# Performance work log

Measured on AMD Instinct MI355X. Metric: run time of the kernel, lower is better.

Reference implementation:

```python
import jax, jax.numpy as jnp
import numpy as np

I1, H1, H2, NC = 38, 50, 15, 14

def _lstm(x, w_ih, w_hh, b_ih, b_hh):
    # x: [B, T, I]; weights in torch layout: w_ih [4H, I], w_hh [4H, H]
    # torch gate order: i, f, g, o
    B, T, _ = x.shape
    H = w_hh.shape[1]
    gx = jnp.einsum('bti,gi->btg', x, w_ih) + b_ih + b_hh  # [B, T, 4H]
    gx = jnp.swapaxes(gx, 0, 1)  # [T, B, 4H]

    def step(carry, g_t):
        h, c = carry
        g = g_t + h @ w_hh.T
        i_g, f_g, c_g, o_g = jnp.split(g, 4, axis=-1)
        i_g = jax.nn.sigmoid(i_g)
        f_g = jax.nn.sigmoid(f_g)
        o_g = jax.nn.sigmoid(o_g)
        c = f_g * c + i_g * jnp.tanh(c_g)
        h = o_g * jnp.tanh(c)
        return (h, c), h

    init = (jnp.zeros((B, H), x.dtype), jnp.zeros((B, H), x.dtype))
    _, hs = jax.lax.scan(step, init, gx)  # hs: [T, B, H]
    return jnp.swapaxes(hs, 0, 1)  # [B, T, H]

def setup_inputs() -> dict:
    key = jax.random.key(0)
    ks = jax.random.split(key, 12)
    s1 = 1.0 / np.sqrt(H1)
    s2 = 1.0 / np.sqrt(H2)
    u = lambda k, shape, s: jax.random.uniform(k, shape, jnp.float32, -s, s)
    return {
        'x': jax.random.normal(ks[0], (4096, 256, I1), jnp.float32),
        'w_ih1': u(ks[1], (4 * H1, I1), s1),
        'w_hh1': u(ks[2], (4 * H1, H1), s1),
        'b_ih1': u(ks[3], (4 * H1,), s1),
        'b_hh1': u(ks[4], (4 * H1,), s1),
        'w_ih2': u(ks[5], (4 * H2, H1), s2),
        'w_hh2': u(ks[6], (4 * H2, H2), s2),
        'b_ih2': u(ks[7], (4 * H2,), s2),
        'b_hh2': u(ks[8], (4 * H2,), s2),
        'w_fc': u(ks[9], (NC, H2), s2),
        'b_fc': u(ks[10], (NC,), s2),
    }

def reference(x, w_ih1, w_hh1, b_ih1, b_hh1, w_ih2, w_hh2, b_ih2, b_hh2, w_fc, b_fc):
    out = _lstm(x, w_ih1, w_hh1, b_ih1, b_hh1)          # [B, T, 50]
    # dropout(0.2) is identity in eval mode
    out = _lstm(out, w_ih2, w_hh2, b_ih2, b_hh2)        # [B, T, 15]
    return out[:, -1, :] @ w_fc.T + b_fc                # [B, 14]
```

## Files before the change

### kernel.cpp

```cpp
#include <hip/hip_runtime.h>


typedef _Float16 f16x8 __attribute__((ext_vector_type(8)));
typedef _Float16 f16x4 __attribute__((ext_vector_type(4)));
typedef float    f32x4 __attribute__((ext_vector_type(4)));

#if __has_builtin(__builtin_amdgcn_exp2f)
#define DEV_EXP2(x) __builtin_amdgcn_exp2f(x)
#else
#define DEV_EXP2(x) exp2f(x)
#endif
#if __has_builtin(__builtin_amdgcn_rcpf)
#define DEV_RCP(x) __builtin_amdgcn_rcpf(x)
#else
#define DEV_RCP(x) (1.0f/(x))
#endif

#define I1 38
#define H1 50
#define H2 15
#define NC 14
#define TT 256
#define SB 16
#define XS 136
#define NTH 512
#define WROW 304
#define L2E 2.885390081777927f
#define L1E 1.442695040888963f

#define MF(A,B,C) __builtin_amdgcn_mfma_f32_16x16x32_f16((A),(B),(C),0,0,0)

__device__ __forceinline__ float sigm(float v)  { return DEV_RCP(1.f + DEV_EXP2(-L1E * v)); }
__device__ __forceinline__ float tanh_f(float v){ return 1.f - 2.f * DEV_RCP(1.f + DEV_EXP2(L2E * v)); }

__launch_bounds__(NTH, 1)
__global__ void lstm2_fused(const float* __restrict__ x,
                            const float* __restrict__ w_ih1, const float* __restrict__ w_hh1,
                            const float* __restrict__ b_ih1, const float* __restrict__ b_hh1,
                            const float* __restrict__ w_ih2, const float* __restrict__ w_hh2,
                            const float* __restrict__ b_ih2, const float* __restrict__ b_hh2,
                            const float* __restrict__ w_fc, const float* __restrict__ b_fc,
                            float* __restrict__ out)
{
  __shared__ __align__(16) _Float16 bufA[2][SB][XS];
  __shared__ __align__(16) _Float16 s_win[2][SB][WROW];

  const int tid  = threadIdx.x;
  const int wv   = tid >> 6;
  const int lane = tid & 63;
  const int lm   = lane & 15;
  const int lk   = lane >> 4;
  const int blk  = blockIdx.x;
  const float* xblk = x + (size_t)blk * SB * TT * I1;

  for (int i = tid; i < 2*SB*XS; i += NTH) ((_Float16*)bufA)[i] = (_Float16)0.f;

  auto welem = [&](bool il1, bool valid, int u, int g, int k) -> _Float16 {
    float w = 0.f;
    if (valid) {
      if (il1) {
        if (k < I1)                w = w_ih1[(g*H1 + u)*I1 + k];
        else if (k < I1 + H1)      w = w_hh1[(g*H1 + u)*H1 + (k - I1)];
      } else {
        if (k >= I1 && k < I1+H1)             w = w_ih2[(g*H2 + u)*H1 + (k - I1)];
        else if (k >= I1+H1 && k < I1+H1+H2)  w = w_hh2[(g*H2 + u)*H2 + (k - I1 - H1)];
      }
    }
    return (_Float16)w;
  };

  const int t1 = wv + 8;
  const int r0 = wv*16 + lm, u0f = r0 >> 2, g0 = r0 & 3;
  const int r1 = t1*16 + lm, q1 = r1 >> 2, g1 = r1 & 3;
  const bool il1f = (q1 < H1);
  const int  u1f = il1f ? q1 : (q1 - H1);
  const bool w16 = (wv == 0);
  const bool c16 = w16 && (lm < 4);

  f16x8 W0[3], W1[4], W16[3];
  #pragma unroll
  for (int ks = 0; ks < 3; ++ks) {
    f16x8 v;
    #pragma unroll
    for (int e = 0; e < 8; ++e) v[e] = welem(true, true, u0f, g0, ks*32 + lk*8 + e);
    W0[ks] = v;
  }
  #pragma unroll
  for (int ks = 0; ks < 4; ++ks) {
    f16x8 v;
    #pragma unroll
    for (int e = 0; e < 8; ++e) v[e] = welem(il1f, true, u1f, g1, ks*32 + lk*8 + e);
    W1[ks] = v;
  }
  #pragma unroll
  for (int j = 0; j < 3; ++j) {
    f16x8 v;
    #pragma unroll
    for (int e = 0; e < 8; ++e) v[e] = welem(false, c16, 14, lm & 3, (j+1)*32 + lk*8 + e);
    W16[j] = v;
  }

  const int uS0 = 4*wv + lk;
  const int d0  = 38 + uS0;
  const int uS1 = 32 + 4*wv + lk;
  const bool il1u = (uS1 < H1);
  const int  uS1r = il1u ? uS1 : (uS1 - H1);
  const int  d1   = il1u ? (38 + uS1) : (88 + uS1r);
  const bool hasC = w16 && (lk == 0);

  float sb0[4], sb1[4], sbC[4];
  #pragma unroll
  for (int m = 0; m < 4; ++m) {
    sb0[m] = b_ih1[m*H1 + uS0] + b_hh1[m*H1 + uS0];
    sb1[m] = il1u ? (b_ih1[m*H1 + uS1] + b_hh1[m*H1 + uS1])
                  : (b_ih2[m*H2 + uS1r] + b_hh2[m*H2 + uS1r]);
    sbC[m] = b_ih2[m*H2 + 14] + b_hh2[m*H2 + 14];
  }

  auto load_window = [&](int t0, int buf) {
    #pragma unroll
    for (int it = 0; it < 3; ++it) {
      int c = it*NTH + tid;
      if (c < SB*76) {
        int s = c / 76, r = c % 76;
        const float4 v = *(const float4*)(xblk + (size_t)s*(TT*I1) + t0*I1 + 4*r);
        f16x4 h;
        h[0] = (_Float16)v.x; h[1] = (_Float16)v.y;
        h[2] = (_Float16)v.z; h[3] = (_Float16)v.w;
        *(f16x4*)&s_win[buf][s][4*r] = h;
      }
    }
  };

  const int e1x = tid + 512;
  const bool v1 = (tid < SB*I1 - 512);
  const int s0 = tid / I1,  k0 = tid % I1;
  const int s1 = e1x / I1,  k1 = e1x % I1;
  const int lb0 = s0*XS + k0, lb1 = v1 ? (s1*XS + k1) : 0;

  load_window(0, 0);
  load_window(8, 1);
  __syncthreads();
  {
    _Float16* b0 = &bufA[0][0][0];
    b0[lb0] = s_win[0][s0][k0];
    if (v1) b0[lb1] = s_win[0][s1][k1];
  }
  __syncthreads();

  float cS0 = 0.f, cS1 = 0.f, cC = 0.f;

  for (int t = 0; t <= TT; ++t) {
    _Float16* cur = &bufA[t & 1][0][0];
    _Float16* nxt = &bufA[(t & 1) ^ 1][0][0];

    if ((t & 7) == 7 && t + 9 < TT)
      load_window(t + 9, ((t + 9) >> 3) & 1);

    f16x8 a0 = *(const f16x8*)(cur + lm*XS +      lk*8);
    f16x8 a1 = *(const f16x8*)(cur + lm*XS + 32 + lk*8);
    f16x8 a2 = *(const f16x8*)(cur + lm*XS + 64 + lk*8);
    f16x8 a3 = *(const f16x8*)(cur + lm*XS + 96 + lk*8);

    {
      f32x4 acc = (f32x4){sb0[0], sb0[1], sb0[2], sb0[3]};
      acc = MF(W0[0], a0, acc);
      acc = MF(W0[1], a1, acc);
      acc = MF(W0[2], a2, acc);
      if (t < TT) {
        float ig = sigm(acc[0]), fg = sigm(acc[1]);
        float gg = tanh_f(acc[2]), og = sigm(acc[3]);
        cS0 = fg*cS0 + ig*gg;
        nxt[lm*XS + d0] = (_Float16)(og * tanh_f(cS0));
      }
    }
    {
      f32x4 acc = (f32x4){sb1[0], sb1[1], sb1[2], sb1[3]};
      acc = MF(W1[0], a0, acc);
      acc = MF(W1[1], a1, acc);
      acc = MF(W1[2], a2, acc);
      acc = MF(W1[3], a3, acc);
      const bool up = il1u ? (t < TT) : (t >= 1);
      if (up) {
        float ig = sigm(acc[0]), fg = sigm(acc[1]);
        float gg = tanh_f(acc[2]), og = sigm(acc[3]);
        cS1 = fg*cS1 + ig*gg;
        nxt[lm*XS + d1] = (_Float16)(og * tanh_f(cS1));
      }
    }
    if (w16) {
      f32x4 acc = (f32x4){sbC[0], sbC[1], sbC[2], sbC[3]};
      acc = MF(W16[0], a1, acc);
      acc = MF(W16[1], a2, acc);
      acc = MF(W16[2], a3, acc);
      if (hasC && t >= 1) {
        float ig = sigm(acc[0]), fg = sigm(acc[1]);
        float gg = tanh_f(acc[2]), og = sigm(acc[3]);
        cC = fg*cC + ig*gg;
        nxt[lm*XS + 102] = (_Float16)(og * tanh_f(cC));
      }
    }

    if (t + 1 < TT) {
      const int tw = (t + 1) & 7, bw = ((t + 1) >> 3) & 1;
      nxt[lb0] = s_win[bw][s0][tw*I1 + k0];
      if (v1) nxt[lb1] = s_win[bw][s1][tw*I1 + k1];
    }

    __syncthreads();
  }

  if (tid < SB*NC) {
    int s = tid / NC, n = tid % NC;
    float acc = b_fc[n];
    #pragma unroll
    for (int u = 0; u < H2; ++u)
      acc += (float)bufA[1][s][88 + u] * w_fc[n*H2 + u];
    out[((size_t)blk*SB + s)*NC + n] = acc;
  }
}

extern "C" void kernel_launch(void* const* d_in, const int* in_sizes, int n_in,
                              void* d_out, int out_size, void* d_ws, size_t ws_size,
                              hipStream_t stream) {
  (void)n_in; (void)d_ws; (void)ws_size; (void)out_size;
  const float* x     = (const float*)d_in[0];
  const float* w_ih1 = (const float*)d_in[1];
  const float* w_hh1 = (const float*)d_in[2];
  const float* b_ih1 = (const float*)d_in[3];
  const float* b_hh1 = (const float*)d_in[4];
  const float* w_ih2 = (const float*)d_in[5];
  const float* w_hh2 = (const float*)d_in[6];
  const float* b_ih2 = (const float*)d_in[7];
  const float* b_hh2 = (const float*)d_in[8];
  const float* w_fc  = (const float*)d_in[9];
  const float* b_fc  = (const float*)d_in[10];
  float* out = (float*)d_out;

  const int B = in_sizes[0] / (TT * I1);
  dim3 grid(B / SB), block(NTH);
  lstm2_fused<<<grid, block, 0, stream>>>(x, w_ih1, w_hh1, b_ih1, b_hh1,
                                          w_ih2, w_hh2, b_ih2, b_hh2,
                                          w_fc, b_fc, out);
}
```

Baseline: 201.8 us.

## Double threads per block, one hidden unit per lane, read x directly from window

The block grows from 512 to 1024 threads, so each wave computes one 16-row gate tile instead of two. This roughly halves the serial MFMA and activation chain per timestep. The per-step copy of x from the staging window into the operand buffer is removed. MFMA A operands are now read straight from a padded x window and a separate hidden-state buffer, and waves skip K-slices that are all zero. The trade-off is more waves synchronising at every step's barrier and the launch bound no longer fixing one block per CU.

```diff
diff --git a/kernel.cpp b/kernel.cpp
--- a/kernel.cpp
+++ b/kernel.cpp
@@ -2,7 +2,7 @@
 
 
 typedef _Float16 f16x8 __attribute__((ext_vector_type(8)));
-typedef _Float16 f16x4 __attribute__((ext_vector_type(4)));
+typedef _Float16 f16x2 __attribute__((ext_vector_type(2)));
 typedef float    f32x4 __attribute__((ext_vector_type(4)));
 
 #if __has_builtin(__builtin_amdgcn_exp2f)
@@ -22,9 +22,12 @@
 #define NC 14
 #define TT 256
 #define SB 16
-#define XS 136
-#define NTH 512
-#define WROW 304
+#define NTH 1024
+#define WSR 328
+#define HS  88
+#define WIN_SZ (2*SB*WSR)
+#define H_OFF  WIN_SZ
+#define SMEM_N (WIN_SZ + 2*SB*HS)
 #define L2E 2.885390081777927f
 #define L1E 1.442695040888963f
 
@@ -33,7 +36,7 @@
 __device__ __forceinline__ float sigm(float v)  { return DEV_RCP(1.f + DEV_EXP2(-L1E * v)); }
 __device__ __forceinline__ float tanh_f(float v){ return 1.f - 2.f * DEV_RCP(1.f + DEV_EXP2(L2E * v)); }
 
-__launch_bounds__(NTH, 1)
+__launch_bounds__(NTH)
 __global__ void lstm2_fused(const float* __restrict__ x,
                             const float* __restrict__ w_ih1, const float* __restrict__ w_hh1,
                             const float* __restrict__ b_ih1, const float* __restrict__ b_hh1,
@@ -42,150 +45,116 @@
                             const float* __restrict__ w_fc, const float* __restrict__ b_fc,
                             float* __restrict__ out)
 {
-  __shared__ __align__(16) _Float16 bufA[2][SB][XS];
-  __shared__ __align__(16) _Float16 s_win[2][SB][WROW];
+  __shared__ __align__(16) _Float16 smem[SMEM_N];
 
   const int tid  = threadIdx.x;
   const int wv   = tid >> 6;
   const int lane = tid & 63;
   const int lm   = lane & 15;
-  const int lk   = lane >> 4;
+  const int lkq  = lane >> 4;
   const int blk  = blockIdx.x;
   const float* xblk = x + (size_t)blk * SB * TT * I1;
 
-  for (int i = tid; i < 2*SB*XS; i += NTH) ((_Float16*)bufA)[i] = (_Float16)0.f;
+  for (int i = tid; i < SMEM_N/2; i += NTH) ((int*)smem)[i] = 0;
 
   auto welem = [&](bool il1, bool valid, int u, int g, int k) -> _Float16 {
     float w = 0.f;
     if (valid) {
       if (il1) {
-        if (k < I1)                w = w_ih1[(g*H1 + u)*I1 + k];
-        else if (k < I1 + H1)      w = w_hh1[(g*H1 + u)*H1 + (k - I1)];
+        if (k < I1)                 w = w_ih1[(g*H1 + u)*I1 + k];
+        else if (k >= 40 && k < 90) w = w_hh1[(g*H1 + u)*H1 + (k - 40)];
       } else {
-        if (k >= I1 && k < I1+H1)             w = w_ih2[(g*H2 + u)*H1 + (k - I1)];
-        else if (k >= I1+H1 && k < I1+H1+H2)  w = w_hh2[(g*H2 + u)*H2 + (k - I1 - H1)];
+        if (k >= 40 && k < 90)        w = w_ih2[(g*H2 + u)*H1 + (k - 40)];
+        else if (k >= 90 && k < 105)  w = w_hh2[(g*H2 + u)*H2 + (k - 90)];
       }
     }
     return (_Float16)w;
   };
 
-  const int t1 = wv + 8;
-  const int r0 = wv*16 + lm, u0f = r0 >> 2, g0 = r0 & 3;
-  const int r1 = t1*16 + lm, q1 = r1 >> 2, g1 = r1 & 3;
-  const bool il1f = (q1 < H1);
-  const int  u1f = il1f ? q1 : (q1 - H1);
-  const bool w16 = (wv == 0);
-  const bool c16 = w16 && (lm < 4);
-
-  f16x8 W0[3], W1[4], W16[3];
-  #pragma unroll
-  for (int ks = 0; ks < 3; ++ks) {
-    f16x8 v;
-    #pragma unroll
-    for (int e = 0; e < 8; ++e) v[e] = welem(true, true, u0f, g0, ks*32 + lk*8 + e);
-    W0[ks] = v;
-  }
+  const int quadW = 4*wv + (lm >> 2);
+  const int gW = lm & 3;
+  const bool il1W = (quadW < H1);
+  const int uW = il1W ? quadW : (quadW - H1);
+
+  f16x8 W[4];
   #pragma unroll
   for (int ks = 0; ks < 4; ++ks) {
     f16x8 v;
     #pragma unroll
-    for (int e = 0; e < 8; ++e) v[e] = welem(il1f, true, u1f, g1, ks*32 + lk*8 + e);
-    W1[ks] = v;
-  }
+    for (int e = 0; e < 8; ++e) v[e] = welem(il1W, true, uW, gW, ks*32 + lkq*8 + e);
+    W[ks] = v;
+  }
+  const bool w16 = (wv == 15);
+  const bool c16 = w16 && (lm < 4);
+  f16x8 W16[3];
   #pragma unroll
   for (int j = 0; j < 3; ++j) {
     f16x8 v;
     #pragma unroll
-    for (int e = 0; e < 8; ++e) v[e] = welem(false, c16, 14, lm & 3, (j+1)*32 + lk*8 + e);
+    for (int e = 0; e < 8; ++e) v[e] = welem(false, c16, 14, lm & 3, (j+1)*32 + lkq*8 + e);
     W16[j] = v;
   }
 
-  const int uS0 = 4*wv + lk;
-  const int d0  = 38 + uS0;
-  const int uS1 = 32 + 4*wv + lk;
-  const bool il1u = (uS1 < H1);
-  const int  uS1r = il1u ? uS1 : (uS1 - H1);
-  const int  d1   = il1u ? (38 + uS1) : (88 + uS1r);
-  const bool hasC = w16 && (lk == 0);
-
-  float sb0[4], sb1[4], sbC[4];
+  const int uU = 4*wv + lkq;
+  const bool il1U = (uU < H1);
+  float sb[4], sbC[4];
   #pragma unroll
   for (int m = 0; m < 4; ++m) {
-    sb0[m] = b_ih1[m*H1 + uS0] + b_hh1[m*H1 + uS0];
-    sb1[m] = il1u ? (b_ih1[m*H1 + uS1] + b_hh1[m*H1 + uS1])
-                  : (b_ih2[m*H2 + uS1r] + b_hh2[m*H2 + uS1r]);
+    sb[m] = il1U ? (b_ih1[m*H1 + uU] + b_hh1[m*H1 + uU])
+                 : (b_ih2[m*H2 + (uU - H1)] + b_hh2[m*H2 + (uU - H1)]);
     sbC[m] = b_ih2[m*H2 + 14] + b_hh2[m*H2 + 14];
   }
 
-  auto load_window = [&](int t0, int buf) {
+  __syncthreads();
+
+  auto fill = [&](int t0, int wb) {
     #pragma unroll
     for (int it = 0; it < 3; ++it) {
-      int c = it*NTH + tid;
-      if (c < SB*76) {
-        int s = c / 76, r = c % 76;
-        const float4 v = *(const float4*)(xblk + (size_t)s*(TT*I1) + t0*I1 + 4*r);
-        f16x4 h;
-        h[0] = (_Float16)v.x; h[1] = (_Float16)v.y;
-        h[2] = (_Float16)v.z; h[3] = (_Float16)v.w;
-        *(f16x4*)&s_win[buf][s][4*r] = h;
+      int e = it*NTH + tid;
+      if (e < SB*152) {
+        int s = e / 152, r = e % 152, tw = r / 19, q = r % 19;
+        const float2 v = *(const float2*)(xblk + (size_t)s*TT*I1 + (t0 + tw)*I1 + 2*q);
+        f16x2 h; h[0] = (_Float16)v.x; h[1] = (_Float16)v.y;
+        *(f16x2*)&smem[wb*(SB*WSR) + s*WSR + tw*40 + 2*q] = h;
       }
     }
   };
-
-  const int e1x = tid + 512;
-  const bool v1 = (tid < SB*I1 - 512);
-  const int s0 = tid / I1,  k0 = tid % I1;
-  const int s1 = e1x / I1,  k1 = e1x % I1;
-  const int lb0 = s0*XS + k0, lb1 = v1 ? (s1*XS + k1) : 0;
-
-  load_window(0, 0);
-  load_window(8, 1);
+  fill(0, 0);
+  fill(8, 1);
   __syncthreads();
-  {
-    _Float16* b0 = &bufA[0][0][0];
-    b0[lb0] = s_win[0][s0][k0];
-    if (v1) b0[lb1] = s_win[0][s1][k1];
-  }
-  __syncthreads();
-
-  float cS0 = 0.f, cS1 = 0.f, cC = 0.f;
+
+  float cU = 0.f, cC = 0.f;
 
   for (int t = 0; t <= TT; ++t) {
-    _Float16* cur = &bufA[t & 1][0][0];
-    _Float16* nxt = &bufA[(t & 1) ^ 1][0][0];
-
-    if ((t & 7) == 7 && t + 9 < TT)
-      load_window(t + 9, ((t + 9) >> 3) & 1);
-
-    f16x8 a0 = *(const f16x8*)(cur + lm*XS +      lk*8);
-    f16x8 a1 = *(const f16x8*)(cur + lm*XS + 32 + lk*8);
-    f16x8 a2 = *(const f16x8*)(cur + lm*XS + 64 + lk*8);
-    f16x8 a3 = *(const f16x8*)(cur + lm*XS + 96 + lk*8);
+    const int par = t & 1;
+    const _Float16* curh = smem + H_OFF + par*(SB*HS);
+    _Float16*       nxth = smem + H_OFF + (par ^ 1)*(SB*HS);
+    const _Float16* wint = smem + ((t >> 3) & 1)*(SB*WSR) + (t & 7)*40;
+
+    if ((t & 7) == 0 && t >= 8 && t + 8 < TT)
+      fill(t + 8, ((t >> 3) + 1) & 1);
+
+    f16x8 a0 = (f16x8)(_Float16)0.f;
+    if (wv <= 12) a0 = *(const f16x8*)(wint + lm*WSR + lkq*8);
+    const _Float16* p1 = lkq ? (curh + lm*HS + (lkq*8 - 8))
+                             : (wint + lm*WSR + 32);
+    f16x8 a1 = *(const f16x8*)p1;
+    f16x8 a2 = *(const f16x8*)(curh + lm*HS + 24 + lkq*8);
+    f16x8 a3 = (f16x8)(_Float16)0.f;
+    if (wv >= 12) a3 = *(const f16x8*)(curh + lm*HS + 56 + lkq*8);
 
     {
-      f32x4 acc = (f32x4){sb0[0], sb0[1], sb0[2], sb0[3]};
-      acc = MF(W0[0], a0, acc);
-      acc = MF(W0[1], a1, acc);
-      acc = MF(W0[2], a2, acc);
-      if (t < TT) {
-        float ig = sigm(acc[0]), fg = sigm(acc[1]);
-        float gg = tanh_f(acc[2]), og = sigm(acc[3]);
-        cS0 = fg*cS0 + ig*gg;
-        nxt[lm*XS + d0] = (_Float16)(og * tanh_f(cS0));
-      }
-    }
-    {
-      f32x4 acc = (f32x4){sb1[0], sb1[1], sb1[2], sb1[3]};
-      acc = MF(W1[0], a0, acc);
-      acc = MF(W1[1], a1, acc);
-      acc = MF(W1[2], a2, acc);
-      acc = MF(W1[3], a3, acc);
-      const bool up = il1u ? (t < TT) : (t >= 1);
+      f32x4 acc = (f32x4){sb[0], sb[1], sb[2], sb[3]};
+      if (wv <= 12) acc = MF(W[0], a0, acc);
+      acc = MF(W[1], a1, acc);
+      acc = MF(W[2], a2, acc);
+      if (wv >= 12) acc = MF(W[3], a3, acc);
+      const bool up = il1U ? (t < TT) : (t >= 1);
       if (up) {
         float ig = sigm(acc[0]), fg = sigm(acc[1]);
         float gg = tanh_f(acc[2]), og = sigm(acc[3]);
-        cS1 = fg*cS1 + ig*gg;
-        nxt[lm*XS + d1] = (_Float16)(og * tanh_f(cS1));
+        cU = fg*cU + ig*gg;
+        nxth[lm*HS + uU] = (_Float16)(og * tanh_f(cU));
       }
     }
     if (w16) {
@@ -193,18 +162,12 @@
       acc = MF(W16[0], a1, acc);
       acc = MF(W16[1], a2, acc);
       acc = MF(W16[2], a3, acc);
-      if (hasC && t >= 1) {
+      if (lkq == 0 && t >= 1) {
         float ig = sigm(acc[0]), fg = sigm(acc[1]);
         float gg = tanh_f(acc[2]), og = sigm(acc[3]);
         cC = fg*cC + ig*gg;
-        nxt[lm*XS + 102] = (_Float16)(og * tanh_f(cC));
-      }
-    }
-
-    if (t + 1 < TT) {
-      const int tw = (t + 1) & 7, bw = ((t + 1) >> 3) & 1;
-      nxt[lb0] = s_win[bw][s0][tw*I1 + k0];
-      if (v1) nxt[lb1] = s_win[bw][s1][tw*I1 + k1];
+        nxth[lm*HS + 64] = (_Float16)(og * tanh_f(cC));
+      }
     }
 
     __syncthreads();
@@ -213,9 +176,10 @@
   if (tid < SB*NC) {
     int s = tid / NC, n = tid % NC;
     float acc = b_fc[n];
+    const _Float16* h2p = smem + H_OFF + (SB*HS) + s*HS + H1;
     #pragma unroll
     for (int u = 0; u < H2; ++u)
-      acc += (float)bufA[1][s][88 + u] * w_fc[n*H2 + u];
+      acc += (float)h2p[u] * w_fc[n*H2 + u];
     out[((size_t)blk*SB + s)*NC + n] = acc;
   }
 }
```

After: 198.7 us. About the same (-1.5%).
